# Optimization experiments

Measured on AMD Instinct MI355X. Metric: run time of the kernel, lower is better.

The kernel has to match this reference:

```python
import jax, jax.numpy as jnp
import numpy as np

D = 256          # d_embed
KD = 256         # key_d_embed
NHEAD = 8
DK = D // NHEAD  # 32
QH = QW = 128
QWS = 16
KH = KW = 64
KWS = 8
R = QWS // KWS   # qk_ratio = 2
SCALE = 1.0 / np.sqrt(DK)


def _rel_index():
    # query coords on fine grid, key coords scaled up by ratio R
    qc = np.stack(np.meshgrid(np.arange(QWS), np.arange(QWS), indexing='ij'), -1).reshape(-1, 2)
    kc = np.stack(np.meshgrid(np.arange(KWS), np.arange(KWS), indexing='ij'), -1).reshape(-1, 2) * R
    rel = qc[:, None, :] - kc[None, :, :] + (QWS - R)  # values in [0, 2*QWS-R-1]
    return jnp.asarray(rel[..., 0] * (2 * QWS - R) + rel[..., 1])  # (QWS^2, KWS^2)


def _partition(t, ws):
    # (B, h, H, W, d) -> (B, h, H/ws, W/ws, ws*ws, d)
    B, h, H, W, d = t.shape
    t = t.reshape(B, h, H // ws, ws, W // ws, ws, d).transpose(0, 1, 2, 4, 3, 5, 6)
    return t.reshape(B, h, H // ws, W // ws, ws * ws, d)


def _merge(t, ws, H, W):
    # inverse of _partition
    B, h, nH, nW, _, d = t.shape
    t = t.reshape(B, h, nH, nW, ws, ws, d).transpose(0, 1, 2, 4, 3, 5, 6)
    return t.reshape(B, h, H, W, d)


def setup_inputs() -> dict:
    key = jax.random.key(0)
    ks = jax.random.split(key, 9)
    x = jax.random.normal(ks[0], (8, QH, QW, D), dtype=jnp.float32)
    z = jax.random.normal(ks[1], (8, KH, KW, KD), dtype=jnp.float32)
    mask = jax.random.randint(ks[2], (1, NHEAD, QH // QWS, QW // QWS, QWS * QWS, KWS * KWS), 0, 2) == 1
    Wq = jax.random.normal(ks[3], (D, D), dtype=jnp.float32) * 0.02
    bq = jnp.zeros((D,), dtype=jnp.float32)
    Wkv = jax.random.normal(ks[4], (KD, 2 * D), dtype=jnp.float32) * 0.02
    bkv = jnp.zeros((2 * D,), dtype=jnp.float32)
    Wo = jax.random.normal(ks[5], (D, D), dtype=jnp.float32) * 0.02
    bo = jnp.zeros((D,), dtype=jnp.float32)
    rel_table = jax.random.normal(ks[6], ((2 * QWS - R) ** 2, NHEAD), dtype=jnp.float32) * 0.02
    return {"x": x, "z": z, "mask": mask, "Wq": Wq, "bq": bq, "Wkv": Wkv, "bkv": bkv, "Wo": Wo, "bo": bo, "rel_table": rel_table}


def reference(x, z, mask, Wq, bq, Wkv, bkv, Wo, bo, rel_table):
    B, H, W, _ = x.shape
    q = (x @ Wq + bq).reshape(B, H, W, NHEAD, DK).transpose(0, 3, 1, 2, 4)        # (B,h,H,W,dk)
    kv = (z @ Wkv + bkv).reshape(B, KH, KW, 2, NHEAD, DK).transpose(3, 0, 4, 1, 2, 5)
    k, v = kv[0], kv[1]                                                           # (B,h,_H,_W,dk)
    sq, sk = QWS // 2, KWS // 2
    q = jnp.roll(q, (-sq, -sq), axis=(2, 3))
    k = jnp.roll(k, (-sk, -sk), axis=(2, 3))
    v = jnp.roll(v, (-sk, -sk), axis=(2, 3))
    q = _partition(q, QWS)   # (B,h,nh,nw,QWS^2,dk)
    k = _partition(k, KWS)   # (B,h,nh,nw,KWS^2,dk)
    v = _partition(v, KWS)
    attn = jnp.einsum('bhnmqd,bhnmkd->bhnmqk', q, k) * SCALE
    bias = rel_table[_rel_index()].transpose(2, 0, 1)[None, :, None, None]        # (1,h,1,1,QWS^2,KWS^2)
    attn = attn + bias
    attn = jnp.where(mask, jnp.float32(-1e9), attn)
    attn = jax.nn.softmax(attn, axis=-1)
    out = jnp.einsum('bhnmqk,bhnmkd->bhnmqd', attn, v)
    out = _merge(out, QWS, H, W)
    out = jnp.roll(out, (sq, sq), axis=(2, 3))
    out = out.transpose(0, 2, 3, 1, 4).reshape(B, H, W, D)
    return out @ Wo + bo
```

## Files before the change

### kernel.cpp

```cpp
#include <hip/hip_runtime.h>
#include <hip/hip_bf16.h>
#include <type_traits>


typedef __attribute__((ext_vector_type(8))) short short8v;
typedef __attribute__((ext_vector_type(4))) float f32x4;
typedef __attribute__((ext_vector_type(8))) unsigned short ushort8v;
typedef unsigned long long u64;

#define DEV __device__ __forceinline__

DEV unsigned short f2bf(float f) {
    union { float f; unsigned u; } v; v.f = f;
    unsigned r = v.u + 0x7FFFu + ((v.u >> 16) & 1u);
    return (unsigned short)(r >> 16);
}

DEV short8v cvt_f32x8(const float4 lo, const float4 hi) {
    union U { __hip_bfloat162 h[4]; short8v s; } u;
    u.h[0] = __float22bfloat162_rn(float2{lo.x, lo.y});
    u.h[1] = __float22bfloat162_rn(float2{lo.z, lo.w});
    u.h[2] = __float22bfloat162_rn(float2{hi.x, hi.y});
    u.h[3] = __float22bfloat162_rn(float2{hi.z, hi.w});
    return u.s;
}

DEV uint2 pack4(f32x4 v) {
    union { __hip_bfloat162 h; unsigned u; } a, b;
    a.h = __float22bfloat162_rn(float2{v[0], v[1]});
    b.h = __float22bfloat162_rn(float2{v[2], v[3]});
    return uint2{a.u, b.u};
}

#define ATT_SCALE 0.17677669529663687f

__global__ void prep_weights(const float* __restrict__ Wq, const float* __restrict__ Wkv,
                             const float* __restrict__ Wo,
                             unsigned short* __restrict__ WqT, unsigned short* __restrict__ WkvT,
                             unsigned short* __restrict__ WoT) {
    int idx = blockIdx.x * 256 + threadIdx.x;
    if (idx < 65536) {
        int n = idx >> 8, k = idx & 255;
        WqT[idx] = f2bf(Wq[k * 256 + n] * ATT_SCALE);
    } else if (idx < 196608) {
        int i = idx - 65536;
        int n = i >> 8, k = i & 255;
        WkvT[i] = f2bf(Wkv[k * 512 + n]);
    } else {
        int i = idx - 196608;
        int n = i >> 8, k = i & 255;
        WoT[i] = f2bf(Wo[k * 256 + n]);
    }
}

__global__ void prep_bias(const float* __restrict__ rel_table, const float* __restrict__ bq,
                          float* __restrict__ biasb, float* __restrict__ bqs) {
    int idx = blockIdx.x * 256 + threadIdx.x;
    if (idx < 131072) {
        int head = idx >> 14;
        int q = (idx >> 6) & 255;
        int k = idx & 63;
        int qi = q >> 4, qj = q & 15;
        int ki = k >> 3, kj = k & 7;
        int r0 = qi - 2 * ki + 14, r1 = qj - 2 * kj + 14;
        biasb[idx] = rel_table[(r0 * 30 + r1) * 8 + head];
    } else if (idx < 131328) {
        int i = idx - 131072;
        bqs[i] = bq[i] * ATT_SCALE;
    }
}

__global__ void prep_mask(const int* __restrict__ mask, u64* __restrict__ mp) {
    int idx = blockIdx.x * 256 + threadIdx.x;
    const int4* src = reinterpret_cast<const int4*>(mask + (size_t)idx * 64);
    u64 bits = 0;
#pragma unroll
    for (int c = 0; c < 16; ++c) {
        int4 v = src[c];
        if (v.x) bits |= 1ull << (c * 4 + 0);
        if (v.y) bits |= 1ull << (c * 4 + 1);
        if (v.z) bits |= 1ull << (c * 4 + 2);
        if (v.w) bits |= 1ull << (c * 4 + 3);
    }
    mp[idx] = bits;
}

__global__ __launch_bounds__(256, 1) void gemm_qrs(
    const float* __restrict__ A,
    const unsigned short* __restrict__ WT,
    const float* __restrict__ bias,
    unsigned short* __restrict__ Cout)
{
    __shared__ __align__(16) unsigned char R[131072];

    const int tid = threadIdx.x;
    const int w = tid >> 6, lane = tid & 63, lr = lane & 15, lg = lane >> 4;
    const int wn = w * 64;
    const size_t rowbase = (size_t)blockIdx.x * 512;

    short8v wf[8][4];
#pragma unroll
    for (int kt = 0; kt < 8; ++kt)
#pragma unroll
        for (int nt = 0; nt < 4; ++nt)
            wf[kt][nt] = *reinterpret_cast<const short8v*>(
                WT + (size_t)(wn + nt * 16 + lr) * 256 + kt * 32 + lg * 8);

    unsigned char* ringbase = R + w * 32768;
    const unsigned char* Ab = (const unsigned char*)A;

    auto issue = [&](int t, int slot) {
        size_t gbyte0 = (rowbase + (size_t)t * 16) * 1024;
        unsigned char* ldst = ringbase + slot * 16384;
#pragma unroll
        for (int r = 0; r < 16; ++r) {
            int v = lane ^ r;
            __builtin_amdgcn_global_load_lds(
                (const __attribute__((address_space(1))) void*)
                    (Ab + gbyte0 + (size_t)r * 1024 + (size_t)v * 16),
                (__attribute__((address_space(3))) void*)(ldst + r * 1024),
                16, 0, 0);
        }
    };

    issue(0, 0);

    for (int t = 0; t < 32; ++t) {
        const int slot = t & 1;
        if (t == 0) asm volatile("s_waitcnt vmcnt(0)" ::: "memory");
        else        asm volatile("s_waitcnt vmcnt(4)" ::: "memory");
        __builtin_amdgcn_sched_barrier(0);

        short8v af[8];
#pragma unroll
        for (int kt = 0; kt < 8; ++kt) {
            int U0 = kt * 8 + lg * 2;
            const unsigned char* base = ringbase + slot * 16384 + lr * 1024;
            float4 f0 = *reinterpret_cast<const float4*>(base + ((U0 ^ lr) << 4));
            float4 f1 = *reinterpret_cast<const float4*>(base + (((U0 + 1) ^ lr) << 4));
            af[kt] = cvt_f32x8(f0, f1);
        }
        __builtin_amdgcn_sched_barrier(0);

        if (t + 1 < 32) issue(t + 1, slot ^ 1);

        f32x4 acc[4];
#pragma unroll
        for (int nt = 0; nt < 4; ++nt) acc[nt] = {0.f, 0.f, 0.f, 0.f};
#pragma unroll
        for (int kt = 0; kt < 8; ++kt)
#pragma unroll
            for (int nt = 0; nt < 4; ++nt)
                acc[nt] = __builtin_amdgcn_mfma_f32_16x16x32_bf16(
                    wf[kt][nt], af[kt], acc[nt], 0, 0, 0);

        size_t row = rowbase + (size_t)t * 16 + lr;
#pragma unroll
        for (int nt = 0; nt < 4; ++nt) {
            f32x4 b4 = *reinterpret_cast<const f32x4*>(bias + wn + nt * 16 + lg * 4);
            *reinterpret_cast<uint2*>(
                Cout + row * 256 + wn + nt * 16 + lg * 4) = pack4(acc[nt] + b4);
        }
    }
}

__global__ __launch_bounds__(512, 2) void gemm_rs(
    const unsigned short* __restrict__ A,
    const unsigned short* __restrict__ WT,
    const float* __restrict__ bias, float* __restrict__ out)
{
    __shared__ __align__(16) unsigned char R[131072];

    const int tid = threadIdx.x;
    const int w = tid >> 6, lane = tid & 63, lr = lane & 15, lg = lane >> 4;
    const int g = w >> 2, wn = (w & 3) * 64;
    const size_t rowbase = (size_t)blockIdx.x * 512 + (size_t)g * 256;

    short8v wf[8][4];
#pragma unroll
    for (int kt = 0; kt < 8; ++kt)
#pragma unroll
        for (int nt = 0; nt < 4; ++nt)
            wf[kt][nt] = *reinterpret_cast<const short8v*>(
                WT + (size_t)(wn + nt * 16 + lr) * 256 + kt * 32 + lg * 8);

    const int r_ = lane >> 5;
    const int u_ = lane & 31;
    unsigned char* ringbase = R + w * 16384;
    const unsigned char* Ab = (const unsigned char*)A;

    auto issue = [&](int t, int slot) {
        size_t gbyte0 = (rowbase + (size_t)t * 16) * 512;
        unsigned char* ldst = ringbase + slot * 8192;
#pragma unroll
        for (int c = 0; c < 8; ++c) {
            int r = 2 * c + r_;
            int v = u_ ^ r;
            __builtin_amdgcn_global_load_lds(
                (const __attribute__((address_space(1))) void*)
                    (Ab + gbyte0 + (size_t)r * 512 + v * 16),
                (__attribute__((address_space(3))) void*)(ldst + c * 1024),
                16, 0, 0);
        }
    };

    issue(0, 0);

    for (int t = 0; t < 16; ++t) {
        const int slot = t & 1;
        if (t == 0) asm volatile("s_waitcnt vmcnt(0)" ::: "memory");
        else        asm volatile("s_waitcnt vmcnt(4)" ::: "memory");
        __builtin_amdgcn_sched_barrier(0);

        short8v af[8];
#pragma unroll
        for (int kt = 0; kt < 8; ++kt)
            af[kt] = *reinterpret_cast<const short8v*>(
                ringbase + slot * 8192 + lr * 512 + (((kt * 4 + lg) ^ lr) << 4));
        __builtin_amdgcn_sched_barrier(0);

        if (t + 1 < 16) issue(t + 1, slot ^ 1);

        f32x4 acc[4];
#pragma unroll
        for (int nt = 0; nt < 4; ++nt) acc[nt] = {0.f, 0.f, 0.f, 0.f};
#pragma unroll
        for (int kt = 0; kt < 8; ++kt)
#pragma unroll
            for (int nt = 0; nt < 4; ++nt)
                acc[nt] = __builtin_amdgcn_mfma_f32_16x16x32_bf16(
                    wf[kt][nt], af[kt], acc[nt], 0, 0, 0);

        size_t row = rowbase + (size_t)t * 16 + lr;
#pragma unroll
        for (int nt = 0; nt < 4; ++nt) {
            f32x4 b4 = *reinterpret_cast<const f32x4*>(bias + wn + nt * 16 + lg * 4);
            *reinterpret_cast<f32x4*>(out + row * 256 + wn + nt * 16 + lg * 4)
                = acc[nt] + b4;
        }
    }
}

template <bool AF32, bool OUT_BF16>
__global__ __launch_bounds__(256) void gemm_proj(
    const void* __restrict__ Ain, const unsigned short* __restrict__ BT,
    const float* __restrict__ bias, void* __restrict__ Cout,
    int M, int N, int K)
{
    __shared__ __align__(16) unsigned char As[2][8192];
    __shared__ __align__(16) unsigned char Bs[2][8192];
    const float* Af = (const float*)Ain;

    const int tid = threadIdx.x;
    const int mb = blockIdx.y * 128, nb = blockIdx.x * 128;
    const int w = tid >> 6, lane = tid & 63, lr = lane & 15, lg = lane >> 4;
    const int wm = (w >> 1) * 64, wn = (w & 1) * 64;

    const int cr0 = (w << 5) + (lane >> 2);
    const int csp = lane & 3;
    const int cs0 = csp ^ ((cr0 >> 1) & 3);
    const int cs1 = csp ^ (((cr0 + 16) >> 1) & 3);

    auto stageB = [&](int buf, int kb) {
        __builtin_amdgcn_global_load_lds(
            (const __attribute__((address_space(1))) void*)(BT + (size_t)(nb + cr0) * K + kb + cs0 * 8),
            (__attribute__((address_space(3))) void*)(&Bs[buf][w << 11]), 16, 0, 0);
        __builtin_amdgcn_global_load_lds(
            (const __attribute__((address_space(1))) void*)(BT + (size_t)(nb + cr0 + 16) * K + kb + cs1 * 8),
            (__attribute__((address_space(3))) void*)(&Bs[buf][(w << 11) + 1024]), 16, 0, 0);
    };

    float4 areg[2][2];
    auto loadA = [&](int kb) {
#pragma unroll
        for (int i = 0; i < 2; ++i) {
            int flat = tid + (i << 8);
            int r = flat >> 2, sp = flat & 3;
            int s = sp ^ ((r >> 1) & 3);
            const float* src = Af + (size_t)(mb + r) * K + kb + s * 8;
            areg[i][0] = *reinterpret_cast<const float4*>(src);
            areg[i][1] = *reinterpret_cast<const float4*>(src + 4);
        }
    };
    auto writeA = [&](int buf) {
#pragma unroll
        for (int i = 0; i < 2; ++i) {
            int flat = tid + (i << 8);
            int r = flat >> 2, sp = flat & 3;
            ushort8v u = { f2bf(areg[i][0].x), f2bf(areg[i][0].y),
                           f2bf(areg[i][0].z), f2bf(areg[i][0].w),
                           f2bf(areg[i][1].x), f2bf(areg[i][1].y),
                           f2bf(areg[i][1].z), f2bf(areg[i][1].w) };
            *reinterpret_cast<ushort8v*>(&As[buf][r * 64 + sp * 16]) = u;
        }
    };
    auto rdA = [&](int buf, int row) -> short8v {
        int swz = (lg ^ ((row >> 1) & 3)) << 4;
        return *reinterpret_cast<const short8v*>(&As[buf][row * 64 + swz]);
    };
    auto rdB = [&](int buf, int row) -> short8v {
        int swz = (lg ^ ((row >> 1) & 3)) << 4;
        return *reinterpret_cast<const short8v*>(&Bs[buf][row * 64 + swz]);
    };

    f32x4 acc[4][4];
#pragma unroll
    for (int i = 0; i < 4; ++i)
#pragma unroll
        for (int j = 0; j < 4; ++j) acc[i][j] = {0.f, 0.f, 0.f, 0.f};

    loadA(0); stageB(0, 0); writeA(0);
    __syncthreads();

    const int NT = K >> 5;
    int cur = 0;
    for (int t = 0; t < NT; ++t) {
        if (t + 1 < NT) { loadA((t + 1) << 5); stageB(cur ^ 1, (t + 1) << 5); }
        short8v af[4], bfr[4];
#pragma unroll
        for (int mt = 0; mt < 4; ++mt) af[mt] = rdA(cur, wm + mt * 16 + lr);
#pragma unroll
        for (int nt = 0; nt < 4; ++nt) bfr[nt] = rdB(cur, wn + nt * 16 + lr);
#pragma unroll
        for (int mt = 0; mt < 4; ++mt)
#pragma unroll
            for (int nt = 0; nt < 4; ++nt)
                acc[mt][nt] = __builtin_amdgcn_mfma_f32_16x16x32_bf16(
                    af[mt], bfr[nt], acc[mt][nt], 0, 0, 0);
        if (t + 1 < NT) writeA(cur ^ 1);
        __syncthreads();
        cur ^= 1;
    }

#pragma unroll
    for (int mt = 0; mt < 4; ++mt)
#pragma unroll
        for (int nt = 0; nt < 4; ++nt)
#pragma unroll
            for (int j = 0; j < 4; ++j) {
                int row = mb + wm + mt * 16 + lg * 4 + j;
                int col = nb + wn + nt * 16 + lr;
                float v = acc[mt][nt][j] + bias[col];
                if constexpr (OUT_BF16)
                    ((unsigned short*)Cout)[(size_t)row * N + col] = f2bf(v);
                else
                    ((float*)Cout)[(size_t)row * N + col] = v;
            }
}

__global__ __launch_bounds__(256) void win_attn(
    unsigned short* __restrict__ Qbuf,
    const unsigned short* __restrict__ KVbuf,
    const u64* __restrict__ maskp,
    const float* __restrict__ biasb)
{
    __shared__ __align__(16) unsigned char Pb[256 * 128];
    __shared__ __align__(16) unsigned short Vt[32][72];

    const int tid = threadIdx.x;
    const int win = blockIdx.x, head = blockIdx.y, b = blockIdx.z;
    const int wi = win >> 3, wj = win & 7;
    const int w = tid >> 6, lane = tid & 63, lr = lane & 15, lg = lane >> 4;
    const int qb = w * 64;

    {
        int key = tid & 63, c = tid >> 6;
        int kr = (wi * 8 + (key >> 3) + 4) & 63;
        int kc = (wj * 8 + (key & 7) + 4) & 63;
        ushort8v v = *reinterpret_cast<const ushort8v*>(
            KVbuf + ((size_t)(b * 4096 + kr * 64 + kc)) * 512 + 256 + head * 32 + c * 8);
#pragma unroll
        for (int e = 0; e < 8; ++e) Vt[c * 8 + e][key] = v[e];
    }

    short8v qf[4], kf[4];
#pragma unroll
    for (int mt = 0; mt < 4; ++mt) {
        int q = qb + mt * 16 + lr;
        int gr = (wi * 16 + (q >> 4) + 8) & 127;
        int gc = (wj * 16 + (q & 15) + 8) & 127;
        qf[mt] = *reinterpret_cast<const short8v*>(
            Qbuf + ((size_t)(b * 16384 + gr * 128 + gc)) * 256 + head * 32 + lg * 8);
    }
#pragma unroll
    for (int nt = 0; nt < 4; ++nt) {
        int key = nt * 16 + lr;
        int kr = (wi * 8 + (key >> 3) + 4) & 63;
        int kc = (wj * 8 + (key & 7) + 4) & 63;
        kf[nt] = *reinterpret_cast<const short8v*>(
            KVbuf + ((size_t)(b * 4096 + kr * 64 + kc)) * 512 + head * 32 + lg * 8);
    }

    f32x4 s[4][4];
#pragma unroll
    for (int mt = 0; mt < 4; ++mt)
#pragma unroll
        for (int nt = 0; nt < 4; ++nt) s[mt][nt] = {0.f, 0.f, 0.f, 0.f};
    __builtin_amdgcn_s_setprio(1);
#pragma unroll
    for (int mt = 0; mt < 4; ++mt)
#pragma unroll
        for (int nt = 0; nt < 4; ++nt)
            s[mt][nt] = __builtin_amdgcn_mfma_f32_16x16x32_bf16(qf[mt], kf[nt], s[mt][nt], 0, 0, 0);
    __builtin_amdgcn_s_setprio(0);

    const u64* mrow = maskp + (size_t)(head * 64 + win) * 256;
#pragma unroll
    for (int mt = 0; mt < 4; ++mt) {
#pragma unroll
        for (int j = 0; j < 4; ++j) {
            int q = qb + mt * 16 + lg * 4 + j;
            u64 mb = mrow[q];
            const float* brow = biasb + (size_t)(head * 256 + q) * 64;
            float v[4];
            float m = -3.0e38f;
#pragma unroll
            for (int nt = 0; nt < 4; ++nt) {
                int key = nt * 16 + lr;
                float sv = s[mt][nt][j] + brow[key];
                if ((mb >> key) & 1ull) sv = -1.0e9f;
                v[nt] = sv;
                m = fmaxf(m, sv);
            }
#pragma unroll
            for (int d = 1; d < 16; d <<= 1) m = fmaxf(m, __shfl_xor(m, d, 64));
            float sum = 0.f;
#pragma unroll
            for (int nt = 0; nt < 4; ++nt) { v[nt] = __expf(v[nt] - m); sum += v[nt]; }
#pragma unroll
            for (int d = 1; d < 16; d <<= 1) sum += __shfl_xor(sum, d, 64);
            float inv = 1.0f / sum;
            int sw = (q & 7) << 4;
#pragma unroll
            for (int nt = 0; nt < 4; ++nt) {
                int off = q * 128 + (((nt * 16 + lr) * 2) ^ sw);
                *reinterpret_cast<unsigned short*>(Pb + off) = f2bf(v[nt] * inv);
            }
        }
    }

    __syncthreads();

    f32x4 o[4][2];
#pragma unroll
    for (int mt = 0; mt < 4; ++mt)
#pragma unroll
        for (int nt = 0; nt < 2; ++nt) o[mt][nt] = {0.f, 0.f, 0.f, 0.f};
#pragma unroll
    for (int kc = 0; kc < 2; ++kc) {
        short8v pf[4], vf[2];
#pragma unroll
        for (int mt = 0; mt < 4; ++mt) {
            int row = qb + mt * 16 + lr;
            int coff = (kc * 64 + lg * 16) ^ ((row & 7) << 4);
            pf[mt] = *reinterpret_cast<const short8v*>(Pb + row * 128 + coff);
        }
#pragma unroll
        for (int nt = 0; nt < 2; ++nt)
            vf[nt] = *reinterpret_cast<const short8v*>(&Vt[nt * 16 + lr][kc * 32 + lg * 8]);
        __builtin_amdgcn_s_setprio(1);
#pragma unroll
        for (int mt = 0; mt < 4; ++mt)
#pragma unroll
            for (int nt = 0; nt < 2; ++nt)
                o[mt][nt] = __builtin_amdgcn_mfma_f32_16x16x32_bf16(pf[mt], vf[nt], o[mt][nt], 0, 0, 0);
        __builtin_amdgcn_s_setprio(0);
    }

#pragma unroll
    for (int mt = 0; mt < 4; ++mt)
#pragma unroll
        for (int j = 0; j < 4; ++j) {
            int q = qb + mt * 16 + lg * 4 + j;
            int gr = (wi * 16 + (q >> 4) + 8) & 127;
            int gc = (wj * 16 + (q & 15) + 8) & 127;
            unsigned short* dst =
                Qbuf + ((size_t)(b * 16384 + gr * 128 + gc)) * 256 + head * 32;
#pragma unroll
            for (int nt = 0; nt < 2; ++nt)
                dst[nt * 16 + lr] = f2bf(o[mt][nt][j]);
        }
}

extern "C" void kernel_launch(void* const* d_in, const int* in_sizes, int n_in,
                              void* d_out, int out_size, void* d_ws, size_t ws_size,
                              hipStream_t stream) {
    const float* x    = (const float*)d_in[0];
    const float* z    = (const float*)d_in[1];
    const int*   mask = (const int*)d_in[2];
    const float* Wq   = (const float*)d_in[3];
    const float* bq   = (const float*)d_in[4];
    const float* Wkv  = (const float*)d_in[5];
    const float* bkv  = (const float*)d_in[6];
    const float* Wo   = (const float*)d_in[7];
    const float* bo   = (const float*)d_in[8];
    const float* rel  = (const float*)d_in[9];
    float* out = (float*)d_out;

    char* ws = (char*)d_ws;
    unsigned short* Qbuf  = (unsigned short*)(ws);
    unsigned short* KVbuf = (unsigned short*)(ws + 67108864);
    unsigned short* WqT   = (unsigned short*)(ws + 100663296);
    unsigned short* WkvT  = (unsigned short*)(ws + 100794368);
    unsigned short* WoT   = (unsigned short*)(ws + 101056512);
    float*          biasb = (float*)(ws + 101187584);
    u64*            maskp = (u64*)(ws + 101711872);
    float*          bqs   = (float*)(ws + 102760448);

    prep_weights<<<1024, 256, 0, stream>>>(Wq, Wkv, Wo, WqT, WkvT, WoT);
    prep_bias<<<513, 256, 0, stream>>>(rel, bq, biasb, bqs);
    prep_mask<<<512, 256, 0, stream>>>(mask, maskp);

    gemm_qrs<<<256, 256, 0, stream>>>(x, WqT, bqs, Qbuf);
    gemm_proj<true, true><<<dim3(4, 256), 256, 0, stream>>>(
        (const void*)z, WkvT, bkv, (void*)KVbuf, 32768, 512, 256);
    win_attn<<<dim3(64, 8, 8), 256, 0, stream>>>(Qbuf, KVbuf, maskp, biasb);
    gemm_rs<<<256, 512, 0, stream>>>(Qbuf, WoT, bo, out);
}
```

Before: 232.4 us.

## Share A tiles across waves with 3-stage LDS ring in Q and O GEMMs

```diff
diff --git a/kernel.cpp b/kernel.cpp
--- a/kernel.cpp
+++ b/kernel.cpp
@@ -85,78 +85,77 @@
     mp[idx] = bits;
 }
 
-__global__ __launch_bounds__(256, 1) void gemm_qrs(
+__global__ __launch_bounds__(512) void gemm_q2(
     const float* __restrict__ A,
     const unsigned short* __restrict__ WT,
     const float* __restrict__ bias,
     unsigned short* __restrict__ Cout)
 {
-    __shared__ __align__(16) unsigned char R[131072];
+    __shared__ __align__(16) unsigned char R[3][16384];
 
     const int tid = threadIdx.x;
     const int w = tid >> 6, lane = tid & 63, lr = lane & 15, lg = lane >> 4;
-    const int wn = w * 64;
-    const size_t rowbase = (size_t)blockIdx.x * 512;
-
-    short8v wf[8][4];
+    const int wn = w * 32;
+    const size_t rowbase = (size_t)blockIdx.x * 256;
+
+    short8v wf[8][2];
 #pragma unroll
     for (int kt = 0; kt < 8; ++kt)
 #pragma unroll
-        for (int nt = 0; nt < 4; ++nt)
+        for (int nt = 0; nt < 2; ++nt)
             wf[kt][nt] = *reinterpret_cast<const short8v*>(
                 WT + (size_t)(wn + nt * 16 + lr) * 256 + kt * 32 + lg * 8);
 
-    unsigned char* ringbase = R + w * 32768;
     const unsigned char* Ab = (const unsigned char*)A;
 
-    auto issue = [&](int t, int slot) {
-        size_t gbyte0 = (rowbase + (size_t)t * 16) * 1024;
-        unsigned char* ldst = ringbase + slot * 16384;
-#pragma unroll
-        for (int r = 0; r < 16; ++r) {
+    auto issue = [&](int t) {
+        int slot = t % 3;
+        size_t g0 = (rowbase + (size_t)t * 16) * 1024;
+#pragma unroll
+        for (int L = 0; L < 2; ++L) {
+            int r = w * 2 + L;
             int v = lane ^ r;
             __builtin_amdgcn_global_load_lds(
                 (const __attribute__((address_space(1))) void*)
-                    (Ab + gbyte0 + (size_t)r * 1024 + (size_t)v * 16),
-                (__attribute__((address_space(3))) void*)(ldst + r * 1024),
+                    (Ab + g0 + (size_t)r * 1024 + (size_t)v * 16),
+                (__attribute__((address_space(3))) void*)(&R[slot][r * 1024]),
                 16, 0, 0);
         }
     };
 
-    issue(0, 0);
-
-    for (int t = 0; t < 32; ++t) {
-        const int slot = t & 1;
-        if (t == 0) asm volatile("s_waitcnt vmcnt(0)" ::: "memory");
-        else        asm volatile("s_waitcnt vmcnt(4)" ::: "memory");
+    issue(0); issue(1);
+
+    for (int t = 0; t < 16; ++t) {
+        if (t == 0)       asm volatile("s_waitcnt vmcnt(2)" ::: "memory");
+        else if (t == 1)  asm volatile("s_waitcnt vmcnt(4)" ::: "memory");
+        else if (t == 15) asm volatile("s_waitcnt vmcnt(4)" ::: "memory");
+        else              asm volatile("s_waitcnt vmcnt(6)" ::: "memory");
+        __builtin_amdgcn_s_barrier();
         __builtin_amdgcn_sched_barrier(0);
 
+        const int slot = t % 3;
         short8v af[8];
 #pragma unroll
         for (int kt = 0; kt < 8; ++kt) {
             int U0 = kt * 8 + lg * 2;
-            const unsigned char* base = ringbase + slot * 16384 + lr * 1024;
+            const unsigned char* base = &R[slot][lr * 1024];
             float4 f0 = *reinterpret_cast<const float4*>(base + ((U0 ^ lr) << 4));
             float4 f1 = *reinterpret_cast<const float4*>(base + (((U0 + 1) ^ lr) << 4));
             af[kt] = cvt_f32x8(f0, f1);
         }
-        __builtin_amdgcn_sched_barrier(0);
-
-        if (t + 1 < 32) issue(t + 1, slot ^ 1);
-
-        f32x4 acc[4];
-#pragma unroll
-        for (int nt = 0; nt < 4; ++nt) acc[nt] = {0.f, 0.f, 0.f, 0.f};
-#pragma unroll
-        for (int kt = 0; kt < 8; ++kt)
-#pragma unroll
-            for (int nt = 0; nt < 4; ++nt)
-                acc[nt] = __builtin_amdgcn_mfma_f32_16x16x32_bf16(
-                    wf[kt][nt], af[kt], acc[nt], 0, 0, 0);
+        if (t + 2 < 16) issue(t + 2);
+
+        f32x4 acc[2];
+        acc[0] = {0.f, 0.f, 0.f, 0.f}; acc[1] = {0.f, 0.f, 0.f, 0.f};
+#pragma unroll
+        for (int kt = 0; kt < 8; ++kt) {
+            acc[0] = __builtin_amdgcn_mfma_f32_16x16x32_bf16(wf[kt][0], af[kt], acc[0], 0, 0, 0);
+            acc[1] = __builtin_amdgcn_mfma_f32_16x16x32_bf16(wf[kt][1], af[kt], acc[1], 0, 0, 0);
+        }
 
         size_t row = rowbase + (size_t)t * 16 + lr;
 #pragma unroll
-        for (int nt = 0; nt < 4; ++nt) {
+        for (int nt = 0; nt < 2; ++nt) {
             f32x4 b4 = *reinterpret_cast<const f32x4*>(bias + wn + nt * 16 + lg * 4);
             *reinterpret_cast<uint2*>(
                 Cout + row * 256 + wn + nt * 16 + lg * 4) = pack4(acc[nt] + b4);
@@ -164,76 +163,71 @@
     }
 }
 
-__global__ __launch_bounds__(512, 2) void gemm_rs(
+__global__ __launch_bounds__(512) void gemm_o2(
     const unsigned short* __restrict__ A,
     const unsigned short* __restrict__ WT,
     const float* __restrict__ bias, float* __restrict__ out)
 {
-    __shared__ __align__(16) unsigned char R[131072];
+    __shared__ __align__(16) unsigned char R[3][8192];
 
     const int tid = threadIdx.x;
     const int w = tid >> 6, lane = tid & 63, lr = lane & 15, lg = lane >> 4;
-    const int g = w >> 2, wn = (w & 3) * 64;
-    const size_t rowbase = (size_t)blockIdx.x * 512 + (size_t)g * 256;
-
-    short8v wf[8][4];
+    const int wn = w * 32;
+    const size_t rowbase = (size_t)blockIdx.x * 256;
+
+    short8v wf[8][2];
 #pragma unroll
     for (int kt = 0; kt < 8; ++kt)
 #pragma unroll
-        for (int nt = 0; nt < 4; ++nt)
+        for (int nt = 0; nt < 2; ++nt)
             wf[kt][nt] = *reinterpret_cast<const short8v*>(
                 WT + (size_t)(wn + nt * 16 + lr) * 256 + kt * 32 + lg * 8);
 
     const int r_ = lane >> 5;
     const int u_ = lane & 31;
-    unsigned char* ringbase = R + w * 16384;
     const unsigned char* Ab = (const unsigned char*)A;
 
-    auto issue = [&](int t, int slot) {
-        size_t gbyte0 = (rowbase + (size_t)t * 16) * 512;
-        unsigned char* ldst = ringbase + slot * 8192;
-#pragma unroll
-        for (int c = 0; c < 8; ++c) {
-            int r = 2 * c + r_;
-            int v = u_ ^ r;
-            __builtin_amdgcn_global_load_lds(
-                (const __attribute__((address_space(1))) void*)
-                    (Ab + gbyte0 + (size_t)r * 512 + v * 16),
-                (__attribute__((address_space(3))) void*)(ldst + c * 1024),
-                16, 0, 0);
-        }
-    };
-
-    issue(0, 0);
+    auto issue = [&](int t) {
+        int slot = t % 3;
+        size_t g0 = (rowbase + (size_t)t * 16) * 512;
+        int r = 2 * w + r_;
+        int v = u_ ^ r;
+        __builtin_amdgcn_global_load_lds(
+            (const __attribute__((address_space(1))) void*)
+                (Ab + g0 + (size_t)r * 512 + (size_t)v * 16),
+            (__attribute__((address_space(3))) void*)(&R[slot][w * 1024]),
+            16, 0, 0);
+    };
+
+    issue(0); issue(1);
 
     for (int t = 0; t < 16; ++t) {
-        const int slot = t & 1;
-        if (t == 0) asm volatile("s_waitcnt vmcnt(0)" ::: "memory");
-        else        asm volatile("s_waitcnt vmcnt(4)" ::: "memory");
+        if (t == 0)       asm volatile("s_waitcnt vmcnt(1)" ::: "memory");
+        else if (t == 1)  asm volatile("s_waitcnt vmcnt(3)" ::: "memory");
+        else if (t == 15) asm volatile("s_waitcnt vmcnt(4)" ::: "memory");
+        else              asm volatile("s_waitcnt vmcnt(5)" ::: "memory");
+        __builtin_amdgcn_s_barrier();
         __builtin_amdgcn_sched_barrier(0);
 
+        const int slot = t % 3;
         short8v af[8];
 #pragma unroll
         for (int kt = 0; kt < 8; ++kt)
             af[kt] = *reinterpret_cast<const short8v*>(
-                ringbase + slot * 8192 + lr * 512 + (((kt * 4 + lg) ^ lr) << 4));
-        __builtin_amdgcn_sched_barrier(0);
-
-        if (t + 1 < 16) issue(t + 1, slot ^ 1);
-
-        f32x4 acc[4];
-#pragma unroll
-        for (int nt = 0; nt < 4; ++nt) acc[nt] = {0.f, 0.f, 0.f, 0.f};
-#pragma unroll
-        for (int kt = 0; kt < 8; ++kt)
-#pragma unroll
-            for (int nt = 0; nt < 4; ++nt)
-                acc[nt] = __builtin_amdgcn_mfma_f32_16x16x32_bf16(
-                    wf[kt][nt], af[kt], acc[nt], 0, 0, 0);
+                &R[slot][lr * 512 + (((kt * 4 + lg) ^ lr) << 4)]);
+        if (t + 2 < 16) issue(t + 2);
+
+        f32x4 acc[2];
+        acc[0] = {0.f, 0.f, 0.f, 0.f}; acc[1] = {0.f, 0.f, 0.f, 0.f};
+#pragma unroll
+        for (int kt = 0; kt < 8; ++kt) {
+            acc[0] = __builtin_amdgcn_mfma_f32_16x16x32_bf16(wf[kt][0], af[kt], acc[0], 0, 0, 0);
+            acc[1] = __builtin_amdgcn_mfma_f32_16x16x32_bf16(wf[kt][1], af[kt], acc[1], 0, 0, 0);
+        }
 
         size_t row = rowbase + (size_t)t * 16 + lr;
 #pragma unroll
-        for (int nt = 0; nt < 4; ++nt) {
+        for (int nt = 0; nt < 2; ++nt) {
             f32x4 b4 = *reinterpret_cast<const f32x4*>(bias + wn + nt * 16 + lg * 4);
             *reinterpret_cast<f32x4*>(out + row * 256 + wn + nt * 16 + lg * 4)
                 = acc[nt] + b4;
@@ -511,9 +505,9 @@
     prep_bias<<<513, 256, 0, stream>>>(rel, bq, biasb, bqs);
     prep_mask<<<512, 256, 0, stream>>>(mask, maskp);
 
-    gemm_qrs<<<256, 256, 0, stream>>>(x, WqT, bqs, Qbuf);
+    gemm_q2<<<512, 512, 0, stream>>>(x, WqT, bqs, Qbuf);
     gemm_proj<true, true><<<dim3(4, 256), 256, 0, stream>>>(
         (const void*)z, WkvT, bkv, (void*)KVbuf, 32768, 512, 256);
     win_attn<<<dim3(64, 8, 8), 256, 0, stream>>>(Qbuf, KVbuf, maskp, biasb);
-    gemm_rs<<<256, 512, 0, stream>>>(Qbuf, WoT, bo, out);
-}
+    gemm_o2<<<512, 512, 0, stream>>>(Qbuf, WoT, bo, out);
+}
```

Measured after the change: 208.5 us, median of 2. 10.3% less time.
